# Performance work log

Hardware: AMD Instinct MI355X
Metric: run time of the kernel (lower is better)

## Reference

```python
import jax, jax.numpy as jnp
import numpy as np

C = 512
G = 2  # num_groups in Normalize default
EPS = 1e-6


def setup_inputs() -> dict:
    key = jax.random.key(0)
    ks = jax.random.split(key, 11)
    B, H, W = 4, 64, 64
    s = 1.0 / np.sqrt(C)
    return {
        "x": jax.random.normal(ks[0], (B, C, H, W), dtype=jnp.float32),
        "gn_w": jnp.ones((C,), jnp.float32),
        "gn_b": jnp.zeros((C,), jnp.float32),
        "wq": jax.random.normal(ks[1], (C, C), jnp.float32) * s,
        "bq": jnp.zeros((C,), jnp.float32),
        "wk": jax.random.normal(ks[2], (C, C), jnp.float32) * s,
        "bk": jnp.zeros((C,), jnp.float32),
        "wv": jax.random.normal(ks[3], (C, C), jnp.float32) * s,
        "bv": jnp.zeros((C,), jnp.float32),
        "wp": jax.random.normal(ks[4], (C, C), jnp.float32) * s,
        "bp": jnp.zeros((C,), jnp.float32),
    }


def _group_norm(x, w, b):
    # x: [B, C, H, W]; GroupNorm over (C//G, H, W) within each group
    B, Cc, H, Wd = x.shape
    xg = x.reshape(B, G, Cc // G, H, Wd)
    mu = jnp.mean(xg, axis=(2, 3, 4), keepdims=True)
    var = jnp.var(xg, axis=(2, 3, 4), keepdims=True)
    xn = (xg - mu) * jax.lax.rsqrt(var + EPS)
    xn = xn.reshape(B, Cc, H, Wd)
    return xn * w[None, :, None, None] + b[None, :, None, None]


def _conv1x1(x, w, b):
    # 1x1 conv == channel matmul. x: [B,C,H,W], w: [O,C]
    return jnp.einsum('bchw,oc->bohw', x, w) + b[None, :, None, None]


def reference(x, gn_w, gn_b, wq, bq, wk, bk, wv, bv, wp, bp):
    B, Cc, H, Wd = x.shape
    h_ = _group_norm(x, gn_w, gn_b)
    q = _conv1x1(h_, wq, bq).reshape(B, Cc, H * Wd)  # [B,C,N]
    k = _conv1x1(h_, wk, bk).reshape(B, Cc, H * Wd)
    v = _conv1x1(h_, wv, bv).reshape(B, Cc, H * Wd)
    # scores: q^T k, scaled by sqrt(C) (NOTE: faithful to source, which
    # multiplies by c**0.5 instead of dividing)
    scale = jnp.sqrt(jnp.float32(Cc)).astype(x.dtype)
    attn = jnp.einsum('bcn,bcm->bnm', q, k) * scale  # [B,N,N]
    attn = jax.nn.softmax(attn, axis=2)
    # h_[b,c,n] = sum_m attn[b,n,m] * v[b,c,m]
    out = jnp.einsum('bnm,bcm->bcn', attn, v).reshape(B, Cc, H, Wd)
    out = _conv1x1(out, wp, bp)
    return x + out
```

## Files before the change

### kernel.cpp

```cpp
#include <hip/hip_runtime.h>
#include <hip/hip_bf16.h>
#include <math.h>

#define B_ 4
#define C_ 512
#define N_ 4096

typedef float f32x4 __attribute__((ext_vector_type(4)));
typedef __bf16 bf16x8 __attribute__((ext_vector_type(8)));

#define AS1(p) ((const __attribute__((address_space(1))) unsigned int*)(p))
#define AS3(p) ((__attribute__((address_space(3))) unsigned int*)(p))

__device__ __forceinline__ unsigned short f2bf(float x){
    return __builtin_bit_cast(unsigned short, (__bf16)x);
}
__device__ __forceinline__ float bf2f(unsigned short b){
    unsigned u = ((unsigned)b)<<16;
    return __builtin_bit_cast(float, u);
}
__device__ __forceinline__ f32x4 mfma16(bf16x8 a, bf16x8 b, f32x4 c){
    return __builtin_amdgcn_mfma_f32_16x16x32_bf16(a, b, c, 0, 0, 0);
}

__global__ void split_w(const float* __restrict__ src, unsigned short* __restrict__ hi,
                        unsigned short* __restrict__ lo){
    const int i = (blockIdx.x*256 + threadIdx.x)*4;
    f32x4 v = *(const f32x4*)(src + i);
    ushort4 h, l;
    unsigned short t0=f2bf(v[0]); h.x=t0; l.x=f2bf(v[0]-bf2f(t0));
    unsigned short t1=f2bf(v[1]); h.y=t1; l.y=f2bf(v[1]-bf2f(t1));
    unsigned short t2=f2bf(v[2]); h.z=t2; l.z=f2bf(v[2]-bf2f(t2));
    unsigned short t3=f2bf(v[3]); h.w=t3; l.w=f2bf(v[3]-bf2f(t3));
    *(ushort4*)(hi + i) = h;
    *(ushort4*)(lo + i) = l;
}

__global__ void gn_part(const float* __restrict__ x, float2* __restrict__ part){
    const int bg = blockIdx.y, blk = blockIdx.x, t = threadIdx.x;
    const float* base = x + (size_t)bg*(256*4096) + (size_t)blk*16384;
    float s = 0.f, q = 0.f;
    for (int i=0;i<16;i++){
        f32x4 v = *(const f32x4*)(base + i*1024 + t*4);
        s += v[0]+v[1]+v[2]+v[3];
        q += v[0]*v[0]+v[1]*v[1]+v[2]*v[2]+v[3]*v[3];
    }
    #pragma unroll
    for (int o=32;o>0;o>>=1){ s += __shfl_down(s, o); q += __shfl_down(q, o); }
    __shared__ float as[4], aq[4];
    if ((t&63)==0){ as[t>>6]=s; aq[t>>6]=q; }
    __syncthreads();
    if (t==0)
        part[bg*64 + blk] = make_float2(as[0]+as[1]+as[2]+as[3], aq[0]+aq[1]+aq[2]+aq[3]);
}

__global__ void gn_fin(const float2* __restrict__ part, float2* __restrict__ stats){
    const int bg = blockIdx.x, t = threadIdx.x;
    float2 p = part[bg*64 + t];
    float s = p.x, q = p.y;
    #pragma unroll
    for (int o=32;o>0;o>>=1){ s += __shfl_down(s,o); q += __shfl_down(q,o); }
    if (t==0){
        const float inv = 1.0f/(256.f*4096.f);
        float mu = s*inv;
        float var = q*inv - mu*mu;
        stats[bg] = make_float2(mu, rsqrtf(var + 1e-6f));
    }
}

__global__ void gn_apply(const float* __restrict__ x, const float* __restrict__ gw,
                         const float* __restrict__ gb, const float2* __restrict__ stats,
                         unsigned short* __restrict__ hTh, unsigned short* __restrict__ hTl)
{
    const int b = blockIdx.z, c0 = blockIdx.y*32, n0 = blockIdx.x*32;
    const int t = threadIdx.x;
    __shared__ float tile[32][37];
    {
        const int cl = t>>3, nl = (t&7)*4;
        const int c = c0 + cl;
        const float2 st = stats[b*2 + (c>>8)];
        const float wv = gw[c], bvv = gb[c];
        const f32x4 v = *(const f32x4*)(x + ((size_t)b*C_ + c)*N_ + n0 + nl);
        #pragma unroll
        for (int i=0;i<4;i++) tile[cl][nl+i] = (v[i] - st.x)*st.y*wv + bvv;
    }
    __syncthreads();
    {
        const int nl = t>>3, cl = (t&7)*4;
        const int n = n0 + nl;
        float f0 = tile[cl+0][nl], f1 = tile[cl+1][nl], f2 = tile[cl+2][nl], f3 = tile[cl+3][nl];
        unsigned short h0=f2bf(f0), h1=f2bf(f1), h2=f2bf(f2), h3=f2bf(f3);
        ushort4 hh, ll;
        hh.x=h0; hh.y=h1; hh.z=h2; hh.w=h3;
        ll.x=f2bf(f0-bf2f(h0)); ll.y=f2bf(f1-bf2f(h1));
        ll.z=f2bf(f2-bf2f(h2)); ll.w=f2bf(f3-bf2f(h3));
        size_t o = ((size_t)b*N_ + n)*C_ + c0 + cl;
        *(ushort4*)(hTh + o) = hh;
        *(ushort4*)(hTl + o) = ll;
    }
}

template<int PROD, int MODE>
__global__ __launch_bounds__(256, 2) void conv_gemm(
    const unsigned short* __restrict__ Wh, const unsigned short* __restrict__ Wl,
    const unsigned short* __restrict__ Sh, const unsigned short* __restrict__ Sl,
    const float* __restrict__ bias,
    unsigned short* __restrict__ outHi, unsigned short* __restrict__ outLo,
    float* __restrict__ outF, const float* __restrict__ resid)
{
    const int b = blockIdx.z, o0 = blockIdx.y*128, n0 = blockIdx.x*128;
    const int t = threadIdx.x, w = t>>6, l = t&63, lr = l&15, lg = l>>4;
    const int ro = (w>>1)*64, co = (w&1)*64;
    __shared__ unsigned short Ah[128][40];
    __shared__ unsigned short Al[128][40];
    __shared__ unsigned short Bh[128][40];
    __shared__ unsigned short Bl[128][40];
    f32x4 acc[4][4];
    #pragma unroll
    for (int i=0;i<4;i++)
        #pragma unroll
        for (int j=0;j<4;j++) acc[i][j] = (f32x4){0.f,0.f,0.f,0.f};

    const size_t srcB = (size_t)b*N_*C_;
    for (int ks=0; ks<16; ks++){
        const int c0 = ks*32;
        #pragma unroll
        for (int i=0;i<2;i++){
            int u = t + i*256;
            int row = u>>2, sch = (u&3)*8;
            *(bf16x8*)&Ah[row][sch] = *(const bf16x8*)(Wh + (size_t)(o0+row)*C_ + c0 + sch);
            *(bf16x8*)&Bh[row][sch] = *(const bf16x8*)(Sh + srcB + (size_t)(n0+row)*C_ + c0 + sch);
            if constexpr (PROD==3){
                *(bf16x8*)&Al[row][sch] = *(const bf16x8*)(Wl + (size_t)(o0+row)*C_ + c0 + sch);
                *(bf16x8*)&Bl[row][sch] = *(const bf16x8*)(Sl + srcB + (size_t)(n0+row)*C_ + c0 + sch);
            }
        }
        __syncthreads();
        bf16x8 af[4], bfv[4], afl[4], bfl[4];
        #pragma unroll
        for (int i=0;i<4;i++){
            af[i]  = *(const bf16x8*)&Ah[ro + i*16 + lr][lg*8];
            bfv[i] = *(const bf16x8*)&Bh[co + i*16 + lr][lg*8];
            if constexpr (PROD==3){
                afl[i] = *(const bf16x8*)&Al[ro + i*16 + lr][lg*8];
                bfl[i] = *(const bf16x8*)&Bl[co + i*16 + lr][lg*8];
            }
        }
        #pragma unroll
        for (int i=0;i<4;i++)
            #pragma unroll
            for (int j=0;j<4;j++){
                acc[i][j] = mfma16(af[i], bfv[j], acc[i][j]);
                if constexpr (PROD==3){
                    acc[i][j] = mfma16(af[i],  bfl[j], acc[i][j]);
                    acc[i][j] = mfma16(afl[i], bfv[j], acc[i][j]);
                }
            }
        __syncthreads();
    }
    #pragma unroll
    for (int i=0;i<4;i++){
        const int ob = o0 + ro + i*16 + lg*4;
        #pragma unroll
        for (int j=0;j<4;j++){
            const int n = n0 + co + j*16 + lr;
            f32x4 v = acc[i][j];
            if constexpr (MODE==0){
                float v0 = v[0] + bias[ob+0]; unsigned short h0 = f2bf(v0);
                float v1 = v[1] + bias[ob+1]; unsigned short h1 = f2bf(v1);
                float v2 = v[2] + bias[ob+2]; unsigned short h2 = f2bf(v2);
                float v3 = v[3] + bias[ob+3]; unsigned short h3 = f2bf(v3);
                ushort4 hh, ll;
                hh.x=h0; hh.y=h1; hh.z=h2; hh.w=h3;
                ll.x=f2bf(v0-bf2f(h0)); ll.y=f2bf(v1-bf2f(h1));
                ll.z=f2bf(v2-bf2f(h2)); ll.w=f2bf(v3-bf2f(h3));
                *(ushort4*)(outHi + srcB + (size_t)n*C_ + ob) = hh;
                *(ushort4*)(outLo + srcB + (size_t)n*C_ + ob) = ll;
            } else if constexpr (MODE==1){
                #pragma unroll
                for (int r=0;r<4;r++)
                    outHi[((size_t)b*C_ + ob + r)*N_ + n] = f2bf(v[r] + bias[ob+r]);
            } else {
                #pragma unroll
                for (int r=0;r<4;r++){
                    size_t idx = ((size_t)b*C_ + ob + r)*N_ + n;
                    outF[idx] = resid[idx] + v[r] + bias[ob+r];
                }
            }
        }
    }
}

__global__ __launch_bounds__(512, 2) void attn_flash4(
    const unsigned short* __restrict__ qTh, const unsigned short* __restrict__ qTl,
    const unsigned short* __restrict__ kTh, const unsigned short* __restrict__ kTl,
    const unsigned short* __restrict__ vB,  unsigned short* __restrict__ aoT)
{
    const int id = blockIdx.x;
    const int xcd = id & 7, slot = id >> 3;
    const int b = xcd >> 1;
    const int n0 = ((xcd & 1)*32 + slot)*64;
    const int t = threadIdx.x, w = t>>6, l = t&63, lr = l&15, lg = l>>4;
    const int fm2 = w>>2, fn = (w>>1)&1, ch = w&1;
    const int cw = w*64;

    __shared__ unsigned short khA[32*512];
    __shared__ unsigned short klA[32*512];
    __shared__ unsigned short khB[32*512];
    __shared__ unsigned short klB[32*512];
    __shared__ float Sb[2][64][33];
    __shared__ __align__(16) unsigned short Pb[64*32];
    __shared__ float rowM[64], rowS[64], rowF[64];

    bf16x8 qh[2][8], ql[2][8];
    #pragma unroll
    for (int f=0; f<2; f++){
        const size_t qr = ((size_t)b*N_ + n0 + fm2*32 + f*16 + lr)*C_ + ch*256;
        #pragma unroll
        for (int kc=0; kc<8; kc++){
            qh[f][kc] = *(const bf16x8*)(qTh + qr + kc*32 + lg*8);
            ql[f][kc] = *(const bf16x8*)(qTl + qr + kc*32 + lg*8);
        }
    }
    f32x4 accO[4][4];
    #pragma unroll
    for (int i=0;i<4;i++)
        #pragma unroll
        for (int j=0;j<4;j++) accO[i][j] = (f32x4){0.f,0.f,0.f,0.f};
    if (t < 64){ rowM[t] = -INFINITY; rowS[t] = 0.f; }

    const size_t kBase = (size_t)b*N_*1024;

    auto stage = [&](int mt, unsigned short* dh, unsigned short* dl){
        const size_t kb = kBase + (size_t)mt*32*1024;
        #pragma unroll
        for (int i=0;i<4;i++){
            const int d = i*8192 + t*16;
            const int row = i*8 + w;
            const int colb = (l*16) ^ ((row&7)<<4);
            const size_t g = kb + (size_t)row*1024 + colb;
            __builtin_amdgcn_global_load_lds(AS1((const char*)kTh + g), AS3((char*)dh + d), 16, 0, 0);
            __builtin_amdgcn_global_load_lds(AS1((const char*)kTl + g), AS3((char*)dl + d), 16, 0, 0);
        }
    };
    auto loadV = [&](int mt, bf16x8* vf){
        const size_t vcol = (size_t)mt*32 + lg*8;
        #pragma unroll
        for (int ac=0;ac<4;ac++)
            vf[ac] = *(const bf16x8*)(vB + ((size_t)b*C_ + cw + ac*16 + lr)*N_ + vcol);
    };
    const float SC = 22.62741699796952f;
    auto qk_tile = [&](const unsigned short* kh, const unsigned short* kl){
        f32x4 s0 = (f32x4){0.f,0.f,0.f,0.f}, s1 = s0;
        const int krow = fn*16 + lr;
        const int rbase = krow*1024;
        const int swz = (krow&7)<<4;
        #pragma unroll
        for (int kc=0;kc<8;kc++){
            const int o = rbase + ((ch*512 + kc*64 + lg*16) ^ swz);
            bf16x8 kf  = *(const bf16x8*)((const char*)kh + o);
            bf16x8 kfl = *(const bf16x8*)((const char*)kl + o);
            s0 = mfma16(qh[0][kc], kf,  s0);
            s0 = mfma16(ql[0][kc], kf,  s0);
            s0 = mfma16(qh[0][kc], kfl, s0);
            s1 = mfma16(qh[1][kc], kf,  s1);
            s1 = mfma16(ql[1][kc], kf,  s1);
            s1 = mfma16(qh[1][kc], kfl, s1);
        }
        #pragma unroll
        for (int r=0;r<4;r++){
            Sb[ch][fm2*32 +      lg*4 + r][fn*16 + lr] = s0[r]*SC;
            Sb[ch][fm2*32 + 16 + lg*4 + r][fn*16 + lr] = s1[r]*SC;
        }
    };

    bf16x8 vf[4];
    loadV(0, vf);
    stage(0, khA, klA);
    asm volatile("s_waitcnt vmcnt(0) lgkmcnt(0)" ::: "memory");
    __builtin_amdgcn_s_barrier();
    stage(1, khB, klB);
    qk_tile(khA, klA);
    asm volatile("s_waitcnt lgkmcnt(0)" ::: "memory");
    __builtin_amdgcn_s_barrier();

    for (int mt=0; mt<128; mt++){
        {
            const int row = t>>3, j = t&7;
            const float* s0p = &Sb[0][row][j*4];
            const float* s1p = &Sb[1][row][j*4];
            float a0 = s0p[0] + s1p[0];
            float a1 = s0p[1] + s1p[1];
            float a2 = s0p[2] + s1p[2];
            float a3 = s0p[3] + s1p[3];
            float mx = fmaxf(fmaxf(a0,a1), fmaxf(a2,a3));
            mx = fmaxf(mx, __shfl_xor(mx, 1, 8));
            mx = fmaxf(mx, __shfl_xor(mx, 2, 8));
            mx = fmaxf(mx, __shfl_xor(mx, 4, 8));
            const float mprev = rowM[row];
            const float mnew = fmaxf(mprev, mx);
            float p0 = __expf(a0 - mnew), p1 = __expf(a1 - mnew);
            float p2 = __expf(a2 - mnew), p3 = __expf(a3 - mnew);
            float ps = (p0+p1)+(p2+p3);
            ps += __shfl_xor(ps, 1, 8);
            ps += __shfl_xor(ps, 2, 8);
            ps += __shfl_xor(ps, 4, 8);
            ushort4 pk; pk.x=f2bf(p0); pk.y=f2bf(p1); pk.z=f2bf(p2); pk.w=f2bf(p3);
            char* pw = (char*)Pb + row*64 + ((((j>>1) + (row>>1)) & 3)<<4) + ((j&1)<<3);
            *(ushort4*)pw = pk;
            if (j==0){
                float f = __expf(mprev - mnew);
                rowF[row] = f;
                rowS[row] = rowS[row]*f + ps;
                rowM[row] = mnew;
            }
        }
        asm volatile("s_waitcnt vmcnt(0) lgkmcnt(0)" ::: "memory");
        __builtin_amdgcn_s_barrier();

        if (mt < 126) stage(mt+2, (mt&1) ? khB : khA, (mt&1) ? klB : klA);
        __builtin_amdgcn_s_setprio(1);
        {
            float frv[4][4]; bool need = false;
            #pragma unroll
            for (int am=0;am<4;am++)
                #pragma unroll
                for (int r=0;r<4;r++){
                    frv[am][r] = rowF[am*16 + lg*4 + r];
                    need |= (frv[am][r] != 1.0f);
                }
            if (__any(need)){
                #pragma unroll
                for (int am=0;am<4;am++)
                    #pragma unroll
                    for (int ac=0;ac<4;ac++)
                        #pragma unroll
                        for (int r=0;r<4;r++) accO[am][ac][r] *= frv[am][r];
            }
            bf16x8 pa[4];
            #pragma unroll
            for (int am=0;am<4;am++){
                const int prow = am*16 + lr;
                pa[am] = *(const bf16x8*)((const char*)Pb + prow*64 + (((lg + (prow>>1)) & 3)<<4));
            }
            #pragma unroll
            for (int ac=0;ac<4;ac++)
                #pragma unroll
                for (int am=0;am<4;am++)
                    accO[am][ac] = mfma16(pa[am], vf[ac], accO[am][ac]);
        }
        if (mt < 127){
            loadV(mt+1, vf);
            qk_tile(((mt+1)&1) ? khB : khA, ((mt+1)&1) ? klB : klA);
        }
        __builtin_amdgcn_s_setprio(0);
        asm volatile("s_waitcnt lgkmcnt(0)" ::: "memory");
        __builtin_amdgcn_s_barrier();
    }

    #pragma unroll
    for (int am=0;am<4;am++)
        #pragma unroll
        for (int r=0;r<4;r++){
            const int n = am*16 + lg*4 + r;
            const float inv = 1.0f / rowS[n];
            #pragma unroll
            for (int ac=0;ac<4;ac++)
                aoT[((size_t)b*N_ + n0 + n)*C_ + cw + ac*16 + lr] = f2bf(accO[am][ac][r]*inv);
        }
}

extern "C" void kernel_launch(void* const* d_in, const int* in_sizes, int n_in,
                              void* d_out, int out_size, void* d_ws, size_t ws_size,
                              hipStream_t stream)
{
    const float* x   = (const float*)d_in[0];
    const float* gnw = (const float*)d_in[1];
    const float* gnb = (const float*)d_in[2];
    const float* wq  = (const float*)d_in[3];
    const float* bq  = (const float*)d_in[4];
    const float* wk  = (const float*)d_in[5];
    const float* bk  = (const float*)d_in[6];
    const float* wv  = (const float*)d_in[7];
    const float* bv  = (const float*)d_in[8];
    const float* wp  = (const float*)d_in[9];
    const float* bp  = (const float*)d_in[10];
    float* out = (float*)d_out;

    char* ws = (char*)d_ws;
    size_t off = 0;
    auto alloc = [&](size_t bytes)->char*{
        char* p = ws + off; off += (bytes + 255) & ~(size_t)255; return p;
    };
    const size_t WB = (size_t)C_*C_*2;
    const size_t TB = (size_t)B_*N_*C_*2;
    unsigned short* wqh = (unsigned short*)alloc(WB);
    unsigned short* wql = (unsigned short*)alloc(WB);
    unsigned short* wkh = (unsigned short*)alloc(WB);
    unsigned short* wkl = (unsigned short*)alloc(WB);
    unsigned short* wvh = (unsigned short*)alloc(WB);
    unsigned short* wvl = (unsigned short*)alloc(WB);
    unsigned short* wph = (unsigned short*)alloc(WB);
    unsigned short* wpl = (unsigned short*)alloc(WB);
    unsigned short* hTh = (unsigned short*)alloc(TB);
    unsigned short* hTl = (unsigned short*)alloc(TB);
    unsigned short* qTh = (unsigned short*)alloc(TB);
    unsigned short* qTl = (unsigned short*)alloc(TB);
    unsigned short* kTh = (unsigned short*)alloc(TB);
    unsigned short* kTl = (unsigned short*)alloc(TB);
    unsigned short* vb  = (unsigned short*)alloc(TB);
    unsigned short* ao  = (unsigned short*)alloc(TB);
    float2* part  = (float2*)alloc(8*64*sizeof(float2));
    float2* stats = (float2*)alloc(8*sizeof(float2));

    split_w<<<256, 256, 0, stream>>>(wq, wqh, wql);
    split_w<<<256, 256, 0, stream>>>(wk, wkh, wkl);
    split_w<<<256, 256, 0, stream>>>(wv, wvh, wvl);
    split_w<<<256, 256, 0, stream>>>(wp, wph, wpl);
    gn_part<<<dim3(64, 8), 256, 0, stream>>>(x, part);
    gn_fin<<<8, 64, 0, stream>>>(part, stats);
    gn_apply<<<dim3(128, 16, B_), 256, 0, stream>>>(x, gnw, gnb, stats, hTh, hTl);
    conv_gemm<3,0><<<dim3(32,4,B_), 256, 0, stream>>>(wqh,wql,hTh,hTl,bq, qTh,qTl,nullptr,nullptr);
    conv_gemm<3,0><<<dim3(32,4,B_), 256, 0, stream>>>(wkh,wkl,hTh,hTl,bk, kTh,kTl,nullptr,nullptr);
    conv_gemm<1,1><<<dim3(32,4,B_), 256, 0, stream>>>(wvh,wvl,hTh,hTl,bv, vb,nullptr,nullptr,nullptr);
    attn_flash4<<<dim3(256), 512, 0, stream>>>(qTh,qTl,kTh,kTl,vb,ao);
    conv_gemm<1,2><<<dim3(32,4,B_), 256, 0, stream>>>(wph,wpl,ao,nullptr,bp, nullptr,nullptr,out,x);
}
```

Measured before the change: 494.9 us.

## Restructure flash attention: per-lane softmax in registers, 32x32 PV MFMA, double-buffered scores

Rewrites the attention kernel so each lane owns one query row's online-softmax state in registers, removing the shared rowM/rowS/rowF and P staging buffers. P·V now uses 32x32x16 MFMAs with P fed directly from registers. Scores are double-buffered so QK of the next tile overlaps softmax/PV of the current tile with one barrier per iteration. K-low is read straight from global instead of staged in LDS, and exp2 with a pre-scaled constant replaces expf. Risks include higher register pressure and uncoalesced global reads for K-low.

```diff
diff --git a/kernel.cpp b/kernel.cpp
--- a/kernel.cpp
+++ b/kernel.cpp
@@ -7,6 +7,7 @@
 #define N_ 4096
 
 typedef float f32x4 __attribute__((ext_vector_type(4)));
+typedef float f32x16 __attribute__((ext_vector_type(16)));
 typedef __bf16 bf16x8 __attribute__((ext_vector_type(8)));
 
 #define AS1(p) ((const __attribute__((address_space(1))) unsigned int*)(p))
@@ -21,6 +22,9 @@
 }
 __device__ __forceinline__ f32x4 mfma16(bf16x8 a, bf16x8 b, f32x4 c){
     return __builtin_amdgcn_mfma_f32_16x16x32_bf16(a, b, c, 0, 0, 0);
+}
+__device__ __forceinline__ f32x16 mfma32(bf16x8 a, bf16x8 b, f32x16 c){
+    return __builtin_amdgcn_mfma_f32_32x32x16_bf16(a, b, c, 0, 0, 0);
 }
 
 __global__ void split_w(const float* __restrict__ src, unsigned short* __restrict__ hi,
@@ -191,7 +195,7 @@
     }
 }
 
-__global__ __launch_bounds__(512, 2) void attn_flash4(
+__global__ __launch_bounds__(512, 2) void attn_flash9(
     const unsigned short* __restrict__ qTh, const unsigned short* __restrict__ qTl,
     const unsigned short* __restrict__ kTh, const unsigned short* __restrict__ kTl,
     const unsigned short* __restrict__ vB,  unsigned short* __restrict__ aoT)
@@ -200,17 +204,13 @@
     const int xcd = id & 7, slot = id >> 3;
     const int b = xcd >> 1;
     const int n0 = ((xcd & 1)*32 + slot)*64;
-    const int t = threadIdx.x, w = t>>6, l = t&63, lr = l&15, lg = l>>4;
+    const int t = threadIdx.x, w = t>>6, l = t&63;
+    const int lr = l&15, lg = l>>4, l31 = l&31, h = l>>5;
     const int fm2 = w>>2, fn = (w>>1)&1, ch = w&1;
-    const int cw = w*64;
-
-    __shared__ unsigned short khA[32*512];
-    __shared__ unsigned short klA[32*512];
-    __shared__ unsigned short khB[32*512];
-    __shared__ unsigned short klB[32*512];
-    __shared__ float Sb[2][64][33];
-    __shared__ __align__(16) unsigned short Pb[64*32];
-    __shared__ float rowM[64], rowS[64], rowF[64];
+    const int nh = w&1, cq = w>>1;
+
+    __shared__ unsigned short khb[2][32*512];
+    __shared__ float Sb[2][2][64][34];
 
     bf16x8 qh[2][8], ql[2][8];
     #pragma unroll
@@ -222,152 +222,138 @@
             ql[f][kc] = *(const bf16x8*)(qTl + qr + kc*32 + lg*8);
         }
     }
-    f32x4 accO[4][4];
-    #pragma unroll
-    for (int i=0;i<4;i++)
-        #pragma unroll
-        for (int j=0;j<4;j++) accO[i][j] = (f32x4){0.f,0.f,0.f,0.f};
-    if (t < 64){ rowM[t] = -INFINITY; rowS[t] = 0.f; }
+    f32x16 accO[4];
+    #pragma unroll
+    for (int i=0;i<4;i++) accO[i] = (f32x16)0.0f;
+    float m_run = -INFINITY, s_run = 0.f;
 
     const size_t kBase = (size_t)b*N_*1024;
-
-    auto stage = [&](int mt, unsigned short* dh, unsigned short* dl){
-        const size_t kb = kBase + (size_t)mt*32*1024;
+    const float SC2 = 32.6444622284f;
+
+    auto stage = [&](int mt, int bi){
+        const size_t kb = kBase + (size_t)mt*32768;
         #pragma unroll
         for (int i=0;i<4;i++){
-            const int d = i*8192 + t*16;
             const int row = i*8 + w;
             const int colb = (l*16) ^ ((row&7)<<4);
-            const size_t g = kb + (size_t)row*1024 + colb;
-            __builtin_amdgcn_global_load_lds(AS1((const char*)kTh + g), AS3((char*)dh + d), 16, 0, 0);
-            __builtin_amdgcn_global_load_lds(AS1((const char*)kTl + g), AS3((char*)dl + d), 16, 0, 0);
+            __builtin_amdgcn_global_load_lds(
+                AS1((const char*)kTh + kb + (size_t)row*1024 + colb),
+                AS3((char*)khb[bi] + row*1024 + l*16), 16, 0, 0);
         }
     };
-    auto loadV = [&](int mt, bf16x8* vf){
-        const size_t vcol = (size_t)mt*32 + lg*8;
-        #pragma unroll
-        for (int ac=0;ac<4;ac++)
-            vf[ac] = *(const bf16x8*)(vB + ((size_t)b*C_ + cw + ac*16 + lr)*N_ + vcol);
+
+    auto qk_tile = [&](int kt, int par){
+        bf16x8 kflv[8];
+        const size_t klrow = ((size_t)b*N_ + (size_t)kt*32 + fn*16 + lr)*C_ + ch*256 + lg*8;
+        #pragma unroll
+        for (int kc=0;kc<8;kc++) kflv[kc] = *(const bf16x8*)(kTl + klrow + kc*32);
+        f32x4 s0 = (f32x4){0.f,0.f,0.f,0.f}, s1 = s0;
+        const char* khB = (const char*)khb[kt&1];
+        const int rbase = (fn*16 + lr)*1024;
+        const int swz = ((fn*16+lr)&7)<<4;
+        #pragma unroll
+        for (int kc=0;kc<8;kc++){
+            bf16x8 kf = *(const bf16x8*)(khB + rbase + ((ch*512 + kc*64 + lg*16) ^ swz));
+            s0 = mfma16(qh[0][kc], kf,       s0);
+            s0 = mfma16(ql[0][kc], kf,       s0);
+            s0 = mfma16(qh[0][kc], kflv[kc], s0);
+            s1 = mfma16(qh[1][kc], kf,       s1);
+            s1 = mfma16(ql[1][kc], kf,       s1);
+            s1 = mfma16(qh[1][kc], kflv[kc], s1);
+        }
+        #pragma unroll
+        for (int r=0;r<4;r++){
+            Sb[par][ch][fm2*32 +      lg*4 + r][fn*16 + lr] = s0[r]*SC2;
+            Sb[par][ch][fm2*32 + 16 + lg*4 + r][fn*16 + lr] = s1[r]*SC2;
+        }
     };
-    const float SC = 22.62741699796952f;
-    auto qk_tile = [&](const unsigned short* kh, const unsigned short* kl){
-        f32x4 s0 = (f32x4){0.f,0.f,0.f,0.f}, s1 = s0;
-        const int krow = fn*16 + lr;
-        const int rbase = krow*1024;
-        const int swz = (krow&7)<<4;
-        #pragma unroll
-        for (int kc=0;kc<8;kc++){
-            const int o = rbase + ((ch*512 + kc*64 + lg*16) ^ swz);
-            bf16x8 kf  = *(const bf16x8*)((const char*)kh + o);
-            bf16x8 kfl = *(const bf16x8*)((const char*)kl + o);
-            s0 = mfma16(qh[0][kc], kf,  s0);
-            s0 = mfma16(ql[0][kc], kf,  s0);
-            s0 = mfma16(qh[0][kc], kfl, s0);
-            s1 = mfma16(qh[1][kc], kf,  s1);
-            s1 = mfma16(ql[1][kc], kf,  s1);
-            s1 = mfma16(qh[1][kc], kfl, s1);
-        }
-        #pragma unroll
-        for (int r=0;r<4;r++){
-            Sb[ch][fm2*32 +      lg*4 + r][fn*16 + lr] = s0[r]*SC;
-            Sb[ch][fm2*32 + 16 + lg*4 + r][fn*16 + lr] = s1[r]*SC;
+
+    auto softmax_pv = [&](int tt){
+        const int par = tt&1;
+        const int nrow = nh*32 + l31;
+        bf16x8 vfa[8];
+        const size_t vrow = ((size_t)b*C_ + cq*128 + l31)*N_ + (size_t)tt*32 + h*8;
+        #pragma unroll
+        for (int cb=0;cb<4;cb++){
+            vfa[cb*2+0] = *(const bf16x8*)(vB + vrow + (size_t)cb*32*N_);
+            vfa[cb*2+1] = *(const bf16x8*)(vB + vrow + (size_t)cb*32*N_ + 16);
+        }
+        const float* r0 = &Sb[par][0][nrow][0];
+        const float* r1 = &Sb[par][1][nrow][0];
+        f32x4 a0 = *(const f32x4*)(r0 + h*8)     + *(const f32x4*)(r1 + h*8);
+        f32x4 a1 = *(const f32x4*)(r0 + h*8 + 4) + *(const f32x4*)(r1 + h*8 + 4);
+        f32x4 a2 = *(const f32x4*)(r0 + 16 + h*8)     + *(const f32x4*)(r1 + 16 + h*8);
+        f32x4 a3 = *(const f32x4*)(r0 + 16 + h*8 + 4) + *(const f32x4*)(r1 + 16 + h*8 + 4);
+        float mx;
+        {
+            f32x4 m01, m23;
+            #pragma unroll
+            for (int i=0;i<4;i++){ m01[i] = fmaxf(a0[i], a1[i]); m23[i] = fmaxf(a2[i], a3[i]); }
+            float m0 = fmaxf(fmaxf(m01[0],m01[1]), fmaxf(m01[2],m01[3]));
+            float m1 = fmaxf(fmaxf(m23[0],m23[1]), fmaxf(m23[2],m23[3]));
+            mx = fmaxf(m0, m1);
+        }
+        mx = fmaxf(mx, __shfl_xor(mx, 32));
+        const float mnew = fmaxf(m_run, mx);
+        const float fsc = exp2f(m_run - mnew);
+        m_run = mnew;
+        float p[16];
+        #pragma unroll
+        for (int i=0;i<4;i++){
+            p[i]    = exp2f(a0[i]-mnew);
+            p[4+i]  = exp2f(a1[i]-mnew);
+            p[8+i]  = exp2f(a2[i]-mnew);
+            p[12+i] = exp2f(a3[i]-mnew);
+        }
+        float ps = ((p[0]+p[1])+(p[2]+p[3])) + ((p[4]+p[5])+(p[6]+p[7]))
+                 + ((p[8]+p[9])+(p[10]+p[11])) + ((p[12]+p[13])+(p[14]+p[15]));
+        ps += __shfl_xor(ps, 32);
+        s_run = s_run*fsc + ps;
+        bf16x8 pa0, pa1;
+        #pragma unroll
+        for (int j=0;j<8;j++){ pa0[j] = (__bf16)p[j]; pa1[j] = (__bf16)p[8+j]; }
+        if (__any(fsc != 1.0f)){
+            #pragma unroll
+            for (int cb=0;cb<4;cb++) accO[cb] *= fsc;
+        }
+        #pragma unroll
+        for (int cb=0;cb<4;cb++){
+            accO[cb] = mfma32(vfa[cb*2+0], pa0, accO[cb]);
+            accO[cb] = mfma32(vfa[cb*2+1], pa1, accO[cb]);
         }
     };
 
-    bf16x8 vf[4];
-    loadV(0, vf);
-    stage(0, khA, klA);
-    asm volatile("s_waitcnt vmcnt(0) lgkmcnt(0)" ::: "memory");
+    stage(0, 0);
+    stage(1, 1);
+    asm volatile("s_waitcnt vmcnt(0)" ::: "memory");
     __builtin_amdgcn_s_barrier();
-    stage(1, khB, klB);
-    qk_tile(khA, klA);
+    qk_tile(0, 0);
     asm volatile("s_waitcnt lgkmcnt(0)" ::: "memory");
     __builtin_amdgcn_s_barrier();
 
-    for (int mt=0; mt<128; mt++){
-        {
-            const int row = t>>3, j = t&7;
-            const float* s0p = &Sb[0][row][j*4];
-            const float* s1p = &Sb[1][row][j*4];
-            float a0 = s0p[0] + s1p[0];
-            float a1 = s0p[1] + s1p[1];
-            float a2 = s0p[2] + s1p[2];
-            float a3 = s0p[3] + s1p[3];
-            float mx = fmaxf(fmaxf(a0,a1), fmaxf(a2,a3));
-            mx = fmaxf(mx, __shfl_xor(mx, 1, 8));
-            mx = fmaxf(mx, __shfl_xor(mx, 2, 8));
-            mx = fmaxf(mx, __shfl_xor(mx, 4, 8));
-            const float mprev = rowM[row];
-            const float mnew = fmaxf(mprev, mx);
-            float p0 = __expf(a0 - mnew), p1 = __expf(a1 - mnew);
-            float p2 = __expf(a2 - mnew), p3 = __expf(a3 - mnew);
-            float ps = (p0+p1)+(p2+p3);
-            ps += __shfl_xor(ps, 1, 8);
-            ps += __shfl_xor(ps, 2, 8);
-            ps += __shfl_xor(ps, 4, 8);
-            ushort4 pk; pk.x=f2bf(p0); pk.y=f2bf(p1); pk.z=f2bf(p2); pk.w=f2bf(p3);
-            char* pw = (char*)Pb + row*64 + ((((j>>1) + (row>>1)) & 3)<<4) + ((j&1)<<3);
-            *(ushort4*)pw = pk;
-            if (j==0){
-                float f = __expf(mprev - mnew);
-                rowF[row] = f;
-                rowS[row] = rowS[row]*f + ps;
-                rowM[row] = mnew;
-            }
-        }
+    for (int tt=0; tt<128; ++tt){
+        if (tt < 126) stage(tt+2, tt&1);
+        if (tt < 127) qk_tile(tt+1, (tt+1)&1);
+        softmax_pv(tt);
         asm volatile("s_waitcnt vmcnt(0) lgkmcnt(0)" ::: "memory");
         __builtin_amdgcn_s_barrier();
-
-        if (mt < 126) stage(mt+2, (mt&1) ? khB : khA, (mt&1) ? klB : klA);
-        __builtin_amdgcn_s_setprio(1);
-        {
-            float frv[4][4]; bool need = false;
+    }
+
+    {
+        const float inv = 1.0f / s_run;
+        const size_t orow = ((size_t)b*N_ + n0 + nh*32 + l31)*C_ + cq*128;
+        #pragma unroll
+        for (int cb=0;cb<4;cb++)
             #pragma unroll
-            for (int am=0;am<4;am++)
-                #pragma unroll
-                for (int r=0;r<4;r++){
-                    frv[am][r] = rowF[am*16 + lg*4 + r];
-                    need |= (frv[am][r] != 1.0f);
-                }
-            if (__any(need)){
-                #pragma unroll
-                for (int am=0;am<4;am++)
-                    #pragma unroll
-                    for (int ac=0;ac<4;ac++)
-                        #pragma unroll
-                        for (int r=0;r<4;r++) accO[am][ac][r] *= frv[am][r];
+            for (int g=0;g<4;g++){
+                ushort4 o;
+                o.x = f2bf(accO[cb][g*4+0]*inv);
+                o.y = f2bf(accO[cb][g*4+1]*inv);
+                o.z = f2bf(accO[cb][g*4+2]*inv);
+                o.w = f2bf(accO[cb][g*4+3]*inv);
+                *(ushort4*)(aoT + orow + cb*32 + g*8 + h*4) = o;
             }
-            bf16x8 pa[4];
-            #pragma unroll
-            for (int am=0;am<4;am++){
-                const int prow = am*16 + lr;
-                pa[am] = *(const bf16x8*)((const char*)Pb + prow*64 + (((lg + (prow>>1)) & 3)<<4));
-            }
-            #pragma unroll
-            for (int ac=0;ac<4;ac++)
-                #pragma unroll
-                for (int am=0;am<4;am++)
-                    accO[am][ac] = mfma16(pa[am], vf[ac], accO[am][ac]);
-        }
-        if (mt < 127){
-            loadV(mt+1, vf);
-            qk_tile(((mt+1)&1) ? khB : khA, ((mt+1)&1) ? klB : klA);
-        }
-        __builtin_amdgcn_s_setprio(0);
-        asm volatile("s_waitcnt lgkmcnt(0)" ::: "memory");
-        __builtin_amdgcn_s_barrier();
-    }
-
-    #pragma unroll
-    for (int am=0;am<4;am++)
-        #pragma unroll
-        for (int r=0;r<4;r++){
-            const int n = am*16 + lg*4 + r;
-            const float inv = 1.0f / rowS[n];
-            #pragma unroll
-            for (int ac=0;ac<4;ac++)
-                aoT[((size_t)b*N_ + n0 + n)*C_ + cw + ac*16 + lr] = f2bf(accO[am][ac][r]*inv);
-        }
+    }
 }
 
 extern "C" void kernel_launch(void* const* d_in, const int* in_sizes, int n_in,
@@ -423,6 +409,6 @@
     conv_gemm<3,0><<<dim3(32,4,B_), 256, 0, stream>>>(wqh,wql,hTh,hTl,bq, qTh,qTl,nullptr,nullptr);
     conv_gemm<3,0><<<dim3(32,4,B_), 256, 0, stream>>>(wkh,wkl,hTh,hTl,bk, kTh,kTl,nullptr,nullptr);
     conv_gemm<1,1><<<dim3(32,4,B_), 256, 0, stream>>>(wvh,wvl,hTh,hTl,bv, vb,nullptr,nullptr,nullptr);
-    attn_flash4<<<dim3(256), 512, 0, stream>>>(qTh,qTl,kTh,kTl,vb,ao);
+    attn_flash9<<<dim3(256), 512, 0, stream>>>(qTh,qTl,kTh,kTl,vb,ao);
     conv_gemm<1,2><<<dim3(32,4,B_), 256, 0, stream>>>(wph,wpl,ao,nullptr,bp, nullptr,nullptr,out,x);
 }
```

Result: slower. 843.4 us (+70.4%).

## Shrink attention tiles to 32 query rows and 16 keys with 256-thread blocks

Applied to the files above, without the earlier changes.

Rewrites the flash-attention kernel so each block handles 32 query rows with 4 waves over 16-key tiles, launching 512 blocks of 256 threads instead of 256 blocks of 512. Softmax now uses exp2 with the log2(e) factor folded into the score scale. V fragments are loaded inside the loop rather than prefetched a tile ahead. The aim is more blocks and lower per-block LDS and register use for better occupancy. In exchange, half of each PV MFMA's K dimension is zero-padded, there are twice as many loop iterations and barriers, and K/V traffic is spread over twice as many blocks.

```diff
diff --git a/kernel.cpp b/kernel.cpp
--- a/kernel.cpp
+++ b/kernel.cpp
@@ -191,7 +191,7 @@
     }
 }
 
-__global__ __launch_bounds__(512, 2) void attn_flash4(
+__global__ __launch_bounds__(256, 2) void attn_flash11(
     const unsigned short* __restrict__ qTh, const unsigned short* __restrict__ qTl,
     const unsigned short* __restrict__ kTh, const unsigned short* __restrict__ kTl,
     const unsigned short* __restrict__ vB,  unsigned short* __restrict__ aoT)
@@ -199,117 +199,99 @@
     const int id = blockIdx.x;
     const int xcd = id & 7, slot = id >> 3;
     const int b = xcd >> 1;
-    const int n0 = ((xcd & 1)*32 + slot)*64;
+    const int n0 = ((xcd & 1)*64 + slot)*32;
     const int t = threadIdx.x, w = t>>6, l = t&63, lr = l&15, lg = l>>4;
-    const int fm2 = w>>2, fn = (w>>1)&1, ch = w&1;
-    const int cw = w*64;
-
-    __shared__ unsigned short khA[32*512];
-    __shared__ unsigned short klA[32*512];
-    __shared__ unsigned short khB[32*512];
-    __shared__ unsigned short klB[32*512];
-    __shared__ float Sb[2][64][33];
-    __shared__ __align__(16) unsigned short Pb[64*32];
-    __shared__ float rowM[64], rowS[64], rowF[64];
-
-    bf16x8 qh[2][8], ql[2][8];
-    #pragma unroll
-    for (int f=0; f<2; f++){
-        const size_t qr = ((size_t)b*N_ + n0 + fm2*32 + f*16 + lr)*C_ + ch*256;
+    const int fm = w>>1, ch = w&1;
+    const int cw = w*128;
+
+    __shared__ unsigned short khb[2][16*512];
+    __shared__ unsigned short klb[2][16*512];
+    __shared__ float Sb[2][32][18];
+    __shared__ __align__(16) unsigned short Pb[32][24];
+    __shared__ float rowM[32], rowS[32], rowF[32];
+
+    bf16x8 qh[8], ql[8];
+    {
+        const size_t qr = ((size_t)b*N_ + n0 + fm*16 + lr)*C_ + ch*256;
         #pragma unroll
         for (int kc=0; kc<8; kc++){
-            qh[f][kc] = *(const bf16x8*)(qTh + qr + kc*32 + lg*8);
-            ql[f][kc] = *(const bf16x8*)(qTl + qr + kc*32 + lg*8);
-        }
-    }
-    f32x4 accO[4][4];
-    #pragma unroll
-    for (int i=0;i<4;i++)
-        #pragma unroll
-        for (int j=0;j<4;j++) accO[i][j] = (f32x4){0.f,0.f,0.f,0.f};
-    if (t < 64){ rowM[t] = -INFINITY; rowS[t] = 0.f; }
+            qh[kc] = *(const bf16x8*)(qTh + qr + kc*32 + lg*8);
+            ql[kc] = *(const bf16x8*)(qTl + qr + kc*32 + lg*8);
+        }
+    }
+    f32x4 accO[2][8];
+    #pragma unroll
+    for (int i=0;i<2;i++)
+        #pragma unroll
+        for (int j=0;j<8;j++) accO[i][j] = (f32x4){0.f,0.f,0.f,0.f};
+    if (t < 32){ rowM[t] = -INFINITY; rowS[t] = 0.f; }
 
     const size_t kBase = (size_t)b*N_*1024;
-
-    auto stage = [&](int mt, unsigned short* dh, unsigned short* dl){
-        const size_t kb = kBase + (size_t)mt*32*1024;
+    const float SC2 = 32.6444622284f;
+
+    auto stage = [&](int mt, int bi){
+        const size_t kb = kBase + (size_t)mt*16*1024;
         #pragma unroll
         for (int i=0;i<4;i++){
-            const int d = i*8192 + t*16;
-            const int row = i*8 + w;
+            const int row = i*4 + w;
             const int colb = (l*16) ^ ((row&7)<<4);
             const size_t g = kb + (size_t)row*1024 + colb;
-            __builtin_amdgcn_global_load_lds(AS1((const char*)kTh + g), AS3((char*)dh + d), 16, 0, 0);
-            __builtin_amdgcn_global_load_lds(AS1((const char*)kTl + g), AS3((char*)dl + d), 16, 0, 0);
+            const int d = bi*16384 + row*1024 + l*16;
+            __builtin_amdgcn_global_load_lds(AS1((const char*)kTh + g), AS3((char*)khb + d), 16, 0, 0);
+            __builtin_amdgcn_global_load_lds(AS1((const char*)kTl + g), AS3((char*)klb + d), 16, 0, 0);
         }
     };
-    auto loadV = [&](int mt, bf16x8* vf){
-        const size_t vcol = (size_t)mt*32 + lg*8;
-        #pragma unroll
-        for (int ac=0;ac<4;ac++)
-            vf[ac] = *(const bf16x8*)(vB + ((size_t)b*C_ + cw + ac*16 + lr)*N_ + vcol);
-    };
-    const float SC = 22.62741699796952f;
-    auto qk_tile = [&](const unsigned short* kh, const unsigned short* kl){
-        f32x4 s0 = (f32x4){0.f,0.f,0.f,0.f}, s1 = s0;
-        const int krow = fn*16 + lr;
-        const int rbase = krow*1024;
-        const int swz = (krow&7)<<4;
+
+    auto qk_tile = [&](int kt){
+        const char* kh = (const char*)khb + (kt&1)*16384;
+        const char* kl = (const char*)klb + (kt&1)*16384;
+        f32x4 s = (f32x4){0.f,0.f,0.f,0.f};
+        const int rbase = lr*1024;
+        const int swz = (lr&7)<<4;
+        __builtin_amdgcn_s_setprio(1);
         #pragma unroll
         for (int kc=0;kc<8;kc++){
             const int o = rbase + ((ch*512 + kc*64 + lg*16) ^ swz);
-            bf16x8 kf  = *(const bf16x8*)((const char*)kh + o);
-            bf16x8 kfl = *(const bf16x8*)((const char*)kl + o);
-            s0 = mfma16(qh[0][kc], kf,  s0);
-            s0 = mfma16(ql[0][kc], kf,  s0);
-            s0 = mfma16(qh[0][kc], kfl, s0);
-            s1 = mfma16(qh[1][kc], kf,  s1);
-            s1 = mfma16(ql[1][kc], kf,  s1);
-            s1 = mfma16(qh[1][kc], kfl, s1);
-        }
-        #pragma unroll
-        for (int r=0;r<4;r++){
-            Sb[ch][fm2*32 +      lg*4 + r][fn*16 + lr] = s0[r]*SC;
-            Sb[ch][fm2*32 + 16 + lg*4 + r][fn*16 + lr] = s1[r]*SC;
-        }
+            bf16x8 kf  = *(const bf16x8*)(kh + o);
+            bf16x8 kfl = *(const bf16x8*)(kl + o);
+            s = mfma16(qh[kc], kf,  s);
+            s = mfma16(ql[kc], kf,  s);
+            s = mfma16(qh[kc], kfl, s);
+        }
+        __builtin_amdgcn_s_setprio(0);
+        #pragma unroll
+        for (int r=0;r<4;r++)
+            Sb[ch][fm*16 + lg*4 + r][lr] = s[r]*SC2;
     };
 
-    bf16x8 vf[4];
-    loadV(0, vf);
-    stage(0, khA, klA);
-    asm volatile("s_waitcnt vmcnt(0) lgkmcnt(0)" ::: "memory");
+    stage(0, 0);
+    stage(1, 1);
+    asm volatile("s_waitcnt vmcnt(0)" ::: "memory");
     __builtin_amdgcn_s_barrier();
-    stage(1, khB, klB);
-    qk_tile(khA, klA);
+    qk_tile(0);
     asm volatile("s_waitcnt lgkmcnt(0)" ::: "memory");
     __builtin_amdgcn_s_barrier();
 
-    for (int mt=0; mt<128; mt++){
+    for (int tt=0; tt<256; ++tt){
         {
             const int row = t>>3, j = t&7;
-            const float* s0p = &Sb[0][row][j*4];
-            const float* s1p = &Sb[1][row][j*4];
-            float a0 = s0p[0] + s1p[0];
-            float a1 = s0p[1] + s1p[1];
-            float a2 = s0p[2] + s1p[2];
-            float a3 = s0p[3] + s1p[3];
-            float mx = fmaxf(fmaxf(a0,a1), fmaxf(a2,a3));
+            float a0 = Sb[0][row][j*2+0] + Sb[1][row][j*2+0];
+            float a1 = Sb[0][row][j*2+1] + Sb[1][row][j*2+1];
+            float mx = fmaxf(a0, a1);
             mx = fmaxf(mx, __shfl_xor(mx, 1, 8));
             mx = fmaxf(mx, __shfl_xor(mx, 2, 8));
             mx = fmaxf(mx, __shfl_xor(mx, 4, 8));
             const float mprev = rowM[row];
             const float mnew = fmaxf(mprev, mx);
-            float p0 = __expf(a0 - mnew), p1 = __expf(a1 - mnew);
-            float p2 = __expf(a2 - mnew), p3 = __expf(a3 - mnew);
-            float ps = (p0+p1)+(p2+p3);
+            float p0 = exp2f(a0 - mnew), p1 = exp2f(a1 - mnew);
+            float ps = p0 + p1;
             ps += __shfl_xor(ps, 1, 8);
             ps += __shfl_xor(ps, 2, 8);
             ps += __shfl_xor(ps, 4, 8);
-            ushort4 pk; pk.x=f2bf(p0); pk.y=f2bf(p1); pk.z=f2bf(p2); pk.w=f2bf(p3);
-            char* pw = (char*)Pb + row*64 + ((((j>>1) + (row>>1)) & 3)<<4) + ((j&1)<<3);
-            *(ushort4*)pw = pk;
+            ushort2 pk; pk.x = f2bf(p0); pk.y = f2bf(p1);
+            *(ushort2*)&Pb[row][j*2] = pk;
             if (j==0){
-                float f = __expf(mprev - mnew);
+                float f = exp2f(mprev - mnew);
                 rowF[row] = f;
                 rowS[row] = rowS[row]*f + ps;
                 rowM[row] = mnew;
@@ -318,12 +300,16 @@
         asm volatile("s_waitcnt vmcnt(0) lgkmcnt(0)" ::: "memory");
         __builtin_amdgcn_s_barrier();
 
-        if (mt < 126) stage(mt+2, (mt&1) ? khB : khA, (mt&1) ? klB : klA);
-        __builtin_amdgcn_s_setprio(1);
+        if (tt < 254) stage(tt+2, tt&1);
         {
-            float frv[4][4]; bool need = false;
-            #pragma unroll
-            for (int am=0;am<4;am++)
+            bf16x8 vf[8];
+            const size_t vcol = (size_t)tt*16 + (lg&1)*8;
+            #pragma unroll
+            for (int cf=0;cf<8;cf++)
+                vf[cf] = *(const bf16x8*)(vB + ((size_t)b*C_ + cw + cf*16 + lr)*N_ + vcol);
+            float frv[2][4]; bool need = false;
+            #pragma unroll
+            for (int am=0;am<2;am++)
                 #pragma unroll
                 for (int r=0;r<4;r++){
                     frv[am][r] = rowF[am*16 + lg*4 + r];
@@ -331,42 +317,40 @@
                 }
             if (__any(need)){
                 #pragma unroll
-                for (int am=0;am<4;am++)
+                for (int am=0;am<2;am++)
                     #pragma unroll
-                    for (int ac=0;ac<4;ac++)
+                    for (int cf=0;cf<8;cf++)
                         #pragma unroll
-                        for (int r=0;r<4;r++) accO[am][ac][r] *= frv[am][r];
-            }
-            bf16x8 pa[4];
-            #pragma unroll
-            for (int am=0;am<4;am++){
-                const int prow = am*16 + lr;
-                pa[am] = *(const bf16x8*)((const char*)Pb + prow*64 + (((lg + (prow>>1)) & 3)<<4));
-            }
-            #pragma unroll
-            for (int ac=0;ac<4;ac++)
+                        for (int r=0;r<4;r++) accO[am][cf][r] *= frv[am][r];
+            }
+            bf16x8 pa[2];
+            #pragma unroll
+            for (int am=0;am<2;am++){
+                if (lg < 2) pa[am] = *(const bf16x8*)&Pb[am*16 + lr][lg*8];
+                else        pa[am] = __builtin_bit_cast(bf16x8, (f32x4){0.f,0.f,0.f,0.f});
+            }
+            __builtin_amdgcn_s_setprio(1);
+            #pragma unroll
+            for (int cf=0;cf<8;cf++)
                 #pragma unroll
-                for (int am=0;am<4;am++)
-                    accO[am][ac] = mfma16(pa[am], vf[ac], accO[am][ac]);
-        }
-        if (mt < 127){
-            loadV(mt+1, vf);
-            qk_tile(((mt+1)&1) ? khB : khA, ((mt+1)&1) ? klB : klA);
-        }
-        __builtin_amdgcn_s_setprio(0);
+                for (int am=0;am<2;am++)
+                    accO[am][cf] = mfma16(pa[am], vf[cf], accO[am][cf]);
+            __builtin_amdgcn_s_setprio(0);
+        }
+        if (tt < 255) qk_tile(tt+1);
         asm volatile("s_waitcnt lgkmcnt(0)" ::: "memory");
         __builtin_amdgcn_s_barrier();
     }
 
     #pragma unroll
-    for (int am=0;am<4;am++)
+    for (int am=0;am<2;am++)
         #pragma unroll
         for (int r=0;r<4;r++){
             const int n = am*16 + lg*4 + r;
             const float inv = 1.0f / rowS[n];
             #pragma unroll
-            for (int ac=0;ac<4;ac++)
-                aoT[((size_t)b*N_ + n0 + n)*C_ + cw + ac*16 + lr] = f2bf(accO[am][ac][r]*inv);
+            for (int cf=0;cf<8;cf++)
+                aoT[((size_t)b*N_ + n0 + n)*C_ + cw + cf*16 + lr] = f2bf(accO[am][cf][r]*inv);
         }
 }
 
@@ -423,6 +407,6 @@
     conv_gemm<3,0><<<dim3(32,4,B_), 256, 0, stream>>>(wqh,wql,hTh,hTl,bq, qTh,qTl,nullptr,nullptr);
     conv_gemm<3,0><<<dim3(32,4,B_), 256, 0, stream>>>(wkh,wkl,hTh,hTl,bk, kTh,kTl,nullptr,nullptr);
     conv_gemm<1,1><<<dim3(32,4,B_), 256, 0, stream>>>(wvh,wvl,hTh,hTl,bv, vb,nullptr,nullptr,nullptr);
-    attn_flash4<<<dim3(256), 512, 0, stream>>>(qTh,qTl,kTh,kTl,vb,ao);
+    attn_flash11<<<dim3(512), 256, 0, stream>>>(qTh,qTl,kTh,kTl,vb,ao);
     conv_gemm<1,2><<<dim3(32,4,B_), 256, 0, stream>>>(wph,wpl,ao,nullptr,bp, nullptr,nullptr,out,x);
 }
```

Measured after the change: 738.0 us. +49.1%, slower.

## Issue K prefetch earlier, fold log2e into scale, vectorize score reads

Applied to the files above, without the earlier changes.

Moves the staging of K tile mt+2 ahead of the softmax step and replaces the full vmcnt(0) wait with a partial vmcnt(8) wait, so global-to-LDS loads overlap the softmax and the barrier. Folds log2(e) into the score scale so softmax can use exp2f instead of __expf. Pads the score buffer to stride 36 with 16-byte alignment so each thread reads its scores as float4. Also raises wave priority around the QK MFMA loop. The partial waitcnt relies on exact in-flight load counts, so a miscount could read stale LDS data.

```diff
diff --git a/kernel.cpp b/kernel.cpp
--- a/kernel.cpp
+++ b/kernel.cpp
@@ -191,7 +191,7 @@
     }
 }
 
-__global__ __launch_bounds__(512, 2) void attn_flash4(
+__global__ __launch_bounds__(512, 2) void attn_flash12(
     const unsigned short* __restrict__ qTh, const unsigned short* __restrict__ qTl,
     const unsigned short* __restrict__ kTh, const unsigned short* __restrict__ kTl,
     const unsigned short* __restrict__ vB,  unsigned short* __restrict__ aoT)
@@ -208,7 +208,7 @@
     __shared__ unsigned short klA[32*512];
     __shared__ unsigned short khB[32*512];
     __shared__ unsigned short klB[32*512];
-    __shared__ float Sb[2][64][33];
+    __shared__ __align__(16) float Sb[2][64][36];
     __shared__ __align__(16) unsigned short Pb[64*32];
     __shared__ float rowM[64], rowS[64], rowF[64];
 
@@ -249,12 +249,13 @@
         for (int ac=0;ac<4;ac++)
             vf[ac] = *(const bf16x8*)(vB + ((size_t)b*C_ + cw + ac*16 + lr)*N_ + vcol);
     };
-    const float SC = 22.62741699796952f;
+    const float SC2 = 32.6444622284f;
     auto qk_tile = [&](const unsigned short* kh, const unsigned short* kl){
         f32x4 s0 = (f32x4){0.f,0.f,0.f,0.f}, s1 = s0;
         const int krow = fn*16 + lr;
         const int rbase = krow*1024;
         const int swz = (krow&7)<<4;
+        __builtin_amdgcn_s_setprio(1);
         #pragma unroll
         for (int kc=0;kc<8;kc++){
             const int o = rbase + ((ch*512 + kc*64 + lg*16) ^ swz);
@@ -267,40 +268,42 @@
             s1 = mfma16(ql[1][kc], kf,  s1);
             s1 = mfma16(qh[1][kc], kfl, s1);
         }
+        __builtin_amdgcn_s_setprio(0);
         #pragma unroll
         for (int r=0;r<4;r++){
-            Sb[ch][fm2*32 +      lg*4 + r][fn*16 + lr] = s0[r]*SC;
-            Sb[ch][fm2*32 + 16 + lg*4 + r][fn*16 + lr] = s1[r]*SC;
+            Sb[ch][fm2*32 +      lg*4 + r][fn*16 + lr] = s0[r]*SC2;
+            Sb[ch][fm2*32 + 16 + lg*4 + r][fn*16 + lr] = s1[r]*SC2;
         }
     };
 
     bf16x8 vf[4];
     loadV(0, vf);
     stage(0, khA, klA);
-    asm volatile("s_waitcnt vmcnt(0) lgkmcnt(0)" ::: "memory");
+    stage(1, khB, klB);
+    asm volatile("s_waitcnt vmcnt(8)" ::: "memory");
     __builtin_amdgcn_s_barrier();
-    stage(1, khB, klB);
     qk_tile(khA, klA);
     asm volatile("s_waitcnt lgkmcnt(0)" ::: "memory");
     __builtin_amdgcn_s_barrier();
 
     for (int mt=0; mt<128; mt++){
+        if (mt < 126) stage(mt+2, (mt&1) ? khB : khA, (mt&1) ? klB : klA);
         {
             const int row = t>>3, j = t&7;
-            const float* s0p = &Sb[0][row][j*4];
-            const float* s1p = &Sb[1][row][j*4];
-            float a0 = s0p[0] + s1p[0];
-            float a1 = s0p[1] + s1p[1];
-            float a2 = s0p[2] + s1p[2];
-            float a3 = s0p[3] + s1p[3];
+            f32x4 u0 = *(const f32x4*)&Sb[0][row][j*4];
+            f32x4 u1 = *(const f32x4*)&Sb[1][row][j*4];
+            float a0 = u0[0] + u1[0];
+            float a1 = u0[1] + u1[1];
+            float a2 = u0[2] + u1[2];
+            float a3 = u0[3] + u1[3];
             float mx = fmaxf(fmaxf(a0,a1), fmaxf(a2,a3));
             mx = fmaxf(mx, __shfl_xor(mx, 1, 8));
             mx = fmaxf(mx, __shfl_xor(mx, 2, 8));
             mx = fmaxf(mx, __shfl_xor(mx, 4, 8));
             const float mprev = rowM[row];
             const float mnew = fmaxf(mprev, mx);
-            float p0 = __expf(a0 - mnew), p1 = __expf(a1 - mnew);
-            float p2 = __expf(a2 - mnew), p3 = __expf(a3 - mnew);
+            float p0 = exp2f(a0 - mnew), p1 = exp2f(a1 - mnew);
+            float p2 = exp2f(a2 - mnew), p3 = exp2f(a3 - mnew);
             float ps = (p0+p1)+(p2+p3);
             ps += __shfl_xor(ps, 1, 8);
             ps += __shfl_xor(ps, 2, 8);
@@ -309,16 +312,16 @@
             char* pw = (char*)Pb + row*64 + ((((j>>1) + (row>>1)) & 3)<<4) + ((j&1)<<3);
             *(ushort4*)pw = pk;
             if (j==0){
-                float f = __expf(mprev - mnew);
+                float f = exp2f(mprev - mnew);
                 rowF[row] = f;
                 rowS[row] = rowS[row]*f + ps;
                 rowM[row] = mnew;
             }
         }
-        asm volatile("s_waitcnt vmcnt(0) lgkmcnt(0)" ::: "memory");
+        if (mt < 126) asm volatile("s_waitcnt vmcnt(8) lgkmcnt(0)" ::: "memory");
+        else          asm volatile("s_waitcnt vmcnt(0) lgkmcnt(0)" ::: "memory");
         __builtin_amdgcn_s_barrier();
 
-        if (mt < 126) stage(mt+2, (mt&1) ? khB : khA, (mt&1) ? klB : klA);
         __builtin_amdgcn_s_setprio(1);
         {
             float frv[4][4]; bool need = false;
@@ -423,6 +426,6 @@
     conv_gemm<3,0><<<dim3(32,4,B_), 256, 0, stream>>>(wqh,wql,hTh,hTl,bq, qTh,qTl,nullptr,nullptr);
     conv_gemm<3,0><<<dim3(32,4,B_), 256, 0, stream>>>(wkh,wkl,hTh,hTl,bk, kTh,kTl,nullptr,nullptr);
     conv_gemm<1,1><<<dim3(32,4,B_), 256, 0, stream>>>(wvh,wvl,hTh,hTl,bv, vb,nullptr,nullptr,nullptr);
-    attn_flash4<<<dim3(256), 512, 0, stream>>>(qTh,qTl,kTh,kTl,vb,ao);
+    attn_flash12<<<dim3(256), 512, 0, stream>>>(qTh,qTl,kTh,kTl,vb,ao);
     conv_gemm<1,2><<<dim3(32,4,B_), 256, 0, stream>>>(wph,wpl,ao,nullptr,bp, nullptr,nullptr,out,x);
 }
```

Result: slower. 544.1 us (+9.9%).
